# Performance work log

Measured on AMD Instinct MI355X. Metric: run time of the kernel, lower is better.

The kernel has to match this reference:

```python
import jax, jax.numpy as jnp
import numpy as np

DIM = 512
NUM_HEADS = 8
HEAD_DIM = DIM // NUM_HEADS
SCALE = HEAD_DIM ** -0.5
B, N = 8, 1024


def setup_inputs() -> dict:
    key = jax.random.key(0)
    k1, k2, k3, k4, k5 = jax.random.split(key, 5)
    x = jax.random.normal(k1, (B, N, DIM), dtype=jnp.float32)
    rpe_bias = jax.random.normal(k2, (1, NUM_HEADS, N, N), dtype=jnp.float32)
    # torch Linear weights: [out_features, in_features], y = x @ W.T
    qkv_w = jax.random.normal(k3, (3 * DIM, DIM), dtype=jnp.float32) * (DIM ** -0.5)
    proj_w = jax.random.normal(k4, (DIM, DIM), dtype=jnp.float32) * (DIM ** -0.5)
    proj_b = jax.random.normal(k5, (DIM,), dtype=jnp.float32) * 0.01
    return {"x": x, "rpe_bias": rpe_bias, "qkv_w": qkv_w, "proj_w": proj_w, "proj_b": proj_b}


def reference(x, rpe_bias, qkv_w, proj_w, proj_b):
    b, n, c = x.shape
    h, d = NUM_HEADS, HEAD_DIM
    # qkv projection (no bias): [B,N,3C] -> [3,B,H,N,D]
    qkv = (x @ qkv_w.T).reshape(b, n, 3, h, d).transpose(2, 0, 3, 1, 4)
    q, k, v = qkv[0], qkv[1], qkv[2]
    attn = jnp.einsum('bhnd,bhmd->bhnm', q, k) * SCALE + rpe_bias
    attn = jax.nn.softmax(attn, axis=-1)  # dropout p=0 -> identity
    out = jnp.einsum('bhnm,bhmd->bhnd', attn, v)
    out = out.transpose(0, 2, 1, 3).reshape(b, n, c)
    return out @ proj_w.T + proj_b
```

## Files before the change

### kernel.cpp

```cpp
#include <hip/hip_runtime.h>
#include <hip/hip_bf16.h>

#define B_    8
#define N_    1024
#define DIM_  512
#define H_    8
#define DH_   64
#define SCALE_ 0.125f

typedef unsigned short u16;
typedef __attribute__((ext_vector_type(8))) short bf16x8;
typedef __attribute__((ext_vector_type(4))) float f32x4;

__device__ __forceinline__ u16 f2bf(float f) {
  union { float f; unsigned u; } v; v.f = f;
  return (u16)((v.u + 0x7fffu + ((v.u >> 16) & 1u)) >> 16);
}
__device__ __forceinline__ unsigned pack2(float a, float b) {
  return (unsigned)f2bf(a) | ((unsigned)f2bf(b) << 16);
}
__device__ __forceinline__ void cp16(const void* g, void* l) {
  __builtin_amdgcn_global_load_lds(
      (const __attribute__((address_space(1))) unsigned*)g,
      (__attribute__((address_space(3))) unsigned*)l, 16, 0, 0);
}

__global__ __launch_bounds__(256) void convert_kernel(
    const float* __restrict__ X, const float* __restrict__ Wq,
    const float* __restrict__ Wp, u16* __restrict__ Xb,
    u16* __restrict__ Wqb, u16* __restrict__ Wpb) {
  const int NX4 = (B_ * N_ * DIM_) / 4;
  const int NQ4 = (3 * DIM_ * DIM_) / 4;
  const int NP4 = (DIM_ * DIM_) / 4;
  const int total = NX4 + NQ4 + NP4;
  const int stride = gridDim.x * 256;
  for (int i = blockIdx.x * 256 + threadIdx.x; i < total; i += stride) {
    const float* s; u16* d; int off;
    if (i < NX4)            { s = X;  d = Xb;  off = i; }
    else if (i < NX4 + NQ4) { s = Wq; d = Wqb; off = i - NX4; }
    else                    { s = Wp; d = Wpb; off = i - NX4 - NQ4; }
    float4 f = *(const float4*)(s + (size_t)off * 4);
    uint2 u; u.x = pack2(f.x, f.y); u.y = pack2(f.z, f.w);
    *(uint2*)(d + (size_t)off * 4) = u;
  }
}

__global__ __launch_bounds__(256) void qkv_gemm(
    const u16* __restrict__ Ab, const u16* __restrict__ Bb,
    u16* __restrict__ Q, u16* __restrict__ K, u16* __restrict__ Vt) {
  __shared__ __align__(16) u16 sA[128 * 64];
  __shared__ __align__(16) u16 sB[128 * 64];
  const int t = threadIdx.x;
  const int wv = t >> 6, lane = t & 63, quad = (lane >> 4) & 3, l15 = lane & 15;
  const int wr = wv >> 1, wc = wv & 1;
  const int m0 = blockIdx.y * 128;
  const int n0 = blockIdx.x * 128;

  const int srow = lane >> 3;
  const int schunk = (lane & 7) ^ srow;
  const size_t ga = (size_t)(m0 + srow) * DIM_ + schunk * 8;
  const size_t gb = (size_t)(n0 + srow) * DIM_ + schunk * 8;

  f32x4 zero = {0.f, 0.f, 0.f, 0.f};
  f32x4 acc[4][4];
#pragma unroll
  for (int i = 0; i < 4; i++)
#pragma unroll
    for (int j = 0; j < 4; j++) acc[i][j] = zero;

  for (int k0 = 0; k0 < DIM_; k0 += 64) {
    __syncthreads();
#pragma unroll
    for (int i = 0; i < 4; i++) {
      const int rb = 32 * wv + 8 * i;
      cp16(Ab + ga + (size_t)rb * DIM_ + k0, &sA[rb * 64]);
      cp16(Bb + gb + (size_t)rb * DIM_ + k0, &sB[rb * 64]);
    }
    __syncthreads();
#pragma unroll
    for (int ks = 0; ks < 2; ks++) {
      bf16x8 af[4], bfv[4];
#pragma unroll
      for (int i = 0; i < 4; i++)
        af[i] = *(const bf16x8*)&sA[(wr * 64 + 16 * i + l15) * 64 +
                                    (((ks << 2) | quad) ^ (l15 & 7)) * 8];
#pragma unroll
      for (int j = 0; j < 4; j++)
        bfv[j] = *(const bf16x8*)&sB[(wc * 64 + 16 * j + l15) * 64 +
                                     (((ks << 2) | quad) ^ (l15 & 7)) * 8];
#pragma unroll
      for (int i = 0; i < 4; i++)
#pragma unroll
        for (int j = 0; j < 4; j++)
          acc[i][j] = __builtin_amdgcn_mfma_f32_16x16x32_bf16(af[i], bfv[j], acc[i][j], 0, 0, 0);
    }
  }

  const int tsel = n0 >> 9;
#pragma unroll
  for (int j = 0; j < 4; j++) {
    const int jg = n0 + wc * 64 + 16 * j + l15;
    const int h = (jg >> 6) & 7, d = jg & 63;
#pragma unroll
    for (int i = 0; i < 4; i++) {
      const int mbase = m0 + wr * 64 + 16 * i + quad * 4;
      const int b = mbase >> 10, nb = mbase & 1023;
      const size_t bh = (size_t)(b * H_ + h);
      if (tsel == 2) {
        ushort4 v4;
        v4.x = f2bf(acc[i][j][0]); v4.y = f2bf(acc[i][j][1]);
        v4.z = f2bf(acc[i][j][2]); v4.w = f2bf(acc[i][j][3]);
        *(ushort4*)&Vt[(bh * DH_ + d) * N_ + nb] = v4;
      } else {
        u16* dst = (tsel == 0 ? Q : K);
#pragma unroll
        for (int rr = 0; rr < 4; rr++)
          dst[(bh * N_ + nb + rr) * DH_ + d] = f2bf(acc[i][j][rr]);
      }
    }
  }
}

__global__ __launch_bounds__(256) void attn_kernel(
    const u16* __restrict__ Q, const u16* __restrict__ K,
    const u16* __restrict__ Vt, const float* __restrict__ bias,
    u16* __restrict__ AO) {
  __shared__ __align__(16) u16 sK[2][64 * 64];
  __shared__ __align__(16) u16 sV[2][64 * 64];
  __shared__ __align__(16) u16 sP[64 * 64];
  const int t = threadIdx.x;
  const int wv = t >> 6, lane = t & 63, quad = (lane >> 4) & 3, l15 = lane & 15;

  const int bid = blockIdx.x;
  const int h = bid & 7;
  const int s = bid >> 3;
  const int nx = s >> 3;
  const int b = s & 7;
  const int n0 = nx << 7;
  const int bh = b * H_ + h;
  const int r = t >> 2, c = (t & 3) << 4;

  const int qgA = n0 + 16 * wv + l15;
  const int qgB = qgA + 64;
  bf16x8 qfA0, qfA1, qfB0, qfB1;
  {
    const u16* qa = Q + (((size_t)bh << 10) + qgA) * DH_ + (quad << 3);
    const u16* qb = Q + (((size_t)bh << 10) + qgB) * DH_ + (quad << 3);
    qfA0 = *(const bf16x8*)qa; qfA1 = *(const bf16x8*)(qa + 32);
    qfB0 = *(const bf16x8*)qb; qfB1 = *(const bf16x8*)(qb + 32);
  }

  const float* bpA = bias + (((size_t)h << 10) + qgA) * N_ + (quad << 2);
  const float* bpB = bias + (((size_t)h << 10) + qgB) * N_ + (quad << 2);
  const u16* kbase = K + (((size_t)bh << 10) + r) * DH_ + c;
  const u16* vbase = Vt + (((size_t)bh << 6) + r) * N_ + c;

  const int so0 = r * 128 + ((((t & 3) << 5)) ^ ((r & 7) << 4));
  const int so1 = r * 128 + ((((t & 3) << 5) + 16) ^ ((r & 7) << 4));
  const int rx = (l15 & 7) << 4;
  const int frow = l15 * 128;
  const int prow = (16 * wv + l15) * 128;

  f32x4 zero = {0.f, 0.f, 0.f, 0.f};
  f32x4 OA[4], OB[4];
#pragma unroll
  for (int i = 0; i < 4; i++) { OA[i] = zero; OB[i] = zero; }
  float lsumA = 0.f, lsumB = 0.f;

  uint4 k0r = *(const uint4*)kbase, k1r = *(const uint4*)(kbase + 8);
  uint4 v0r = *(const uint4*)vbase, v1r = *(const uint4*)(vbase + 8);
  *(uint4*)((char*)sK[0] + so0) = k0r; *(uint4*)((char*)sK[0] + so1) = k1r;
  *(uint4*)((char*)sV[0] + so0) = v0r; *(uint4*)((char*)sV[0] + so1) = v1r;
  {
    const u16* kn = kbase + (size_t)64 * DH_;
    const u16* vn = vbase + 64;
    k0r = *(const uint4*)kn; k1r = *(const uint4*)(kn + 8);
    v0r = *(const uint4*)vn; v1r = *(const uint4*)(vn + 8);
  }
  __syncthreads();

  for (int kt = 0; kt < 16; kt++) {
    const u16* cK = sK[kt & 1];
    const u16* cV = sV[kt & 1];
    if (kt < 15) {
      u16* wK = sK[(kt & 1) ^ 1]; u16* wV = sV[(kt & 1) ^ 1];
      *(uint4*)((char*)wK + so0) = k0r; *(uint4*)((char*)wK + so1) = k1r;
      *(uint4*)((char*)wV + so0) = v0r; *(uint4*)((char*)wV + so1) = v1r;
      if (kt < 14) {
        const u16* kn = kbase + (size_t)(kt + 2) * 64 * DH_;
        const u16* vn = vbase + (kt + 2) * 64;
        k0r = *(const uint4*)kn; k1r = *(const uint4*)(kn + 8);
        v0r = *(const uint4*)vn; v1r = *(const uint4*)(vn + 8);
      }
    }
    float4 bA[4], bB[4];
#pragma unroll
    for (int cb = 0; cb < 4; cb++) {
      bA[cb] = *(const float4*)(bpA + (kt << 6) + 16 * cb);
      bB[cb] = *(const float4*)(bpB + (kt << 6) + 16 * cb);
    }

    bf16x8 kf[8];
#pragma unroll
    for (int ks = 0; ks < 2; ks++)
#pragma unroll
      for (int cb = 0; cb < 4; cb++)
        kf[ks * 4 + cb] = *(const bf16x8*)((const char*)cK + cb * 2048 + frow +
                                           (((ks << 6) | (quad << 4)) ^ rx));

    f32x4 SA[4], SB[4];
#pragma unroll
    for (int i = 0; i < 4; i++) { SA[i] = zero; SB[i] = zero; }
    __builtin_amdgcn_s_setprio(1);
#pragma unroll
    for (int ks = 0; ks < 2; ks++) {
      const bf16x8 qa = ks ? qfA1 : qfA0;
      const bf16x8 qb = ks ? qfB1 : qfB0;
#pragma unroll
      for (int cb = 0; cb < 4; cb++) {
        SA[cb] = __builtin_amdgcn_mfma_f32_16x16x32_bf16(kf[ks * 4 + cb], qa, SA[cb], 0, 0, 0);
        SB[cb] = __builtin_amdgcn_mfma_f32_16x16x32_bf16(kf[ks * 4 + cb], qb, SB[cb], 0, 0, 0);
      }
    }
    __builtin_amdgcn_s_setprio(0);

#pragma unroll
    for (int cb = 0; cb < 4; cb++) {
      float p0 = __expf(fmaf(SA[cb][0], SCALE_, bA[cb].x));
      float p1 = __expf(fmaf(SA[cb][1], SCALE_, bA[cb].y));
      float p2 = __expf(fmaf(SA[cb][2], SCALE_, bA[cb].z));
      float p3 = __expf(fmaf(SA[cb][3], SCALE_, bA[cb].w));
      lsumA += (p0 + p1) + (p2 + p3);
      uint2 pk; pk.x = pack2(p0, p1); pk.y = pack2(p2, p3);
      *(uint2*)((char*)sP + prow + (((cb << 5) | (quad << 3)) ^ rx)) = pk;
    }
    bf16x8 vf[8];
#pragma unroll
    for (int ks = 0; ks < 2; ks++)
#pragma unroll
      for (int cb = 0; cb < 4; cb++)
        vf[ks * 4 + cb] = *(const bf16x8*)((const char*)cV + cb * 2048 + frow +
                                           (((ks << 6) | (quad << 4)) ^ rx));
    asm volatile("s_waitcnt lgkmcnt(0)" ::: "memory");

    __builtin_amdgcn_s_setprio(1);
#pragma unroll
    for (int ks = 0; ks < 2; ks++) {
      bf16x8 pf = *(const bf16x8*)((const char*)sP + prow +
                                   (((ks << 6) | (quad << 4)) ^ rx));
#pragma unroll
      for (int cb = 0; cb < 4; cb++)
        OA[cb] = __builtin_amdgcn_mfma_f32_16x16x32_bf16(vf[ks * 4 + cb], pf, OA[cb], 0, 0, 0);
    }
    __builtin_amdgcn_s_setprio(0);

#pragma unroll
    for (int cb = 0; cb < 4; cb++) {
      float p0 = __expf(fmaf(SB[cb][0], SCALE_, bB[cb].x));
      float p1 = __expf(fmaf(SB[cb][1], SCALE_, bB[cb].y));
      float p2 = __expf(fmaf(SB[cb][2], SCALE_, bB[cb].z));
      float p3 = __expf(fmaf(SB[cb][3], SCALE_, bB[cb].w));
      lsumB += (p0 + p1) + (p2 + p3);
      uint2 pk; pk.x = pack2(p0, p1); pk.y = pack2(p2, p3);
      *(uint2*)((char*)sP + prow + (((cb << 5) | (quad << 3)) ^ rx)) = pk;
    }
    asm volatile("s_waitcnt lgkmcnt(0)" ::: "memory");
    __builtin_amdgcn_s_setprio(1);
#pragma unroll
    for (int ks = 0; ks < 2; ks++) {
      bf16x8 pf = *(const bf16x8*)((const char*)sP + prow +
                                   (((ks << 6) | (quad << 4)) ^ rx));
#pragma unroll
      for (int cb = 0; cb < 4; cb++)
        OB[cb] = __builtin_amdgcn_mfma_f32_16x16x32_bf16(vf[ks * 4 + cb], pf, OB[cb], 0, 0, 0);
    }
    __builtin_amdgcn_s_setprio(0);
    __syncthreads();
  }

  lsumA += __shfl_xor(lsumA, 16); lsumA += __shfl_xor(lsumA, 32);
  lsumB += __shfl_xor(lsumB, 16); lsumB += __shfl_xor(lsumB, 32);
  const float invA = 1.f / lsumA, invB = 1.f / lsumB;
#pragma unroll
  for (int cb = 0; cb < 4; cb++) {
    ushort4 o4;
    o4.x = f2bf(OA[cb][0] * invA); o4.y = f2bf(OA[cb][1] * invA);
    o4.z = f2bf(OA[cb][2] * invA); o4.w = f2bf(OA[cb][3] * invA);
    *(ushort4*)&AO[(((size_t)b << 10) + qgA) * DIM_ + h * DH_ + 16 * cb + (quad << 2)] = o4;
    ushort4 p4;
    p4.x = f2bf(OB[cb][0] * invB); p4.y = f2bf(OB[cb][1] * invB);
    p4.z = f2bf(OB[cb][2] * invB); p4.w = f2bf(OB[cb][3] * invB);
    *(ushort4*)&AO[(((size_t)b << 10) + qgB) * DIM_ + h * DH_ + 16 * cb + (quad << 2)] = p4;
  }
}

__global__ __launch_bounds__(256) void proj_gemm(
    const u16* __restrict__ Ab, const u16* __restrict__ Bb,
    const float* __restrict__ Pb, float* __restrict__ Out) {
  __shared__ __align__(16) u16 sA[128 * 64];
  __shared__ __align__(16) u16 sB[128 * 64];
  const int t = threadIdx.x;
  const int wv = t >> 6, lane = t & 63, quad = (lane >> 4) & 3, l15 = lane & 15;
  const int wr = wv >> 1, wc = wv & 1;
  const int m0 = blockIdx.y * 128;
  const int n0 = blockIdx.x * 128;

  const int srow = lane >> 3;
  const int schunk = (lane & 7) ^ srow;
  const size_t ga = (size_t)(m0 + srow) * DIM_ + schunk * 8;
  const size_t gb = (size_t)(n0 + srow) * DIM_ + schunk * 8;

  f32x4 zero = {0.f, 0.f, 0.f, 0.f};
  f32x4 acc[4][4];
#pragma unroll
  for (int i = 0; i < 4; i++)
#pragma unroll
    for (int j = 0; j < 4; j++) acc[i][j] = zero;

  for (int k0 = 0; k0 < DIM_; k0 += 64) {
    __syncthreads();
#pragma unroll
    for (int i = 0; i < 4; i++) {
      const int rb = 32 * wv + 8 * i;
      cp16(Ab + ga + (size_t)rb * DIM_ + k0, &sA[rb * 64]);
      cp16(Bb + gb + (size_t)rb * DIM_ + k0, &sB[rb * 64]);
    }
    __syncthreads();
#pragma unroll
    for (int ks = 0; ks < 2; ks++) {
      bf16x8 af[4], bfv[4];
#pragma unroll
      for (int i = 0; i < 4; i++)
        af[i] = *(const bf16x8*)&sA[(wr * 64 + 16 * i + l15) * 64 +
                                    (((ks << 2) | quad) ^ (l15 & 7)) * 8];
#pragma unroll
      for (int j = 0; j < 4; j++)
        bfv[j] = *(const bf16x8*)&sB[(wc * 64 + 16 * j + l15) * 64 +
                                     (((ks << 2) | quad) ^ (l15 & 7)) * 8];
#pragma unroll
      for (int i = 0; i < 4; i++)
#pragma unroll
        for (int j = 0; j < 4; j++)
          acc[i][j] = __builtin_amdgcn_mfma_f32_16x16x32_bf16(af[i], bfv[j], acc[i][j], 0, 0, 0);
    }
  }

#pragma unroll
  for (int j = 0; j < 4; j++) {
    const int jg = n0 + wc * 64 + 16 * j + l15;
    const float pb = Pb[jg];
#pragma unroll
    for (int i = 0; i < 4; i++) {
      const int mbase = m0 + wr * 64 + 16 * i + quad * 4;
#pragma unroll
      for (int rr = 0; rr < 4; rr++)
        Out[(size_t)(mbase + rr) * DIM_ + jg] = acc[i][j][rr] + pb;
    }
  }
}

extern "C" void kernel_launch(void* const* d_in, const int* in_sizes, int n_in,
                              void* d_out, int out_size, void* d_ws, size_t ws_size,
                              hipStream_t stream) {
  const float* x      = (const float*)d_in[0];
  const float* rpe    = (const float*)d_in[1];
  const float* qkv_w  = (const float*)d_in[2];
  const float* proj_w = (const float*)d_in[3];
  const float* proj_b = (const float*)d_in[4];
  float* out = (float*)d_out;

  const size_t perbuf = (size_t)B_ * N_ * DIM_;
  u16* Xb  = (u16*)d_ws;
  u16* Q   = Xb + perbuf;
  u16* K   = Q + perbuf;
  u16* Vt  = K + perbuf;
  u16* Wqb = Vt + perbuf;
  u16* Wpb = Wqb + (size_t)3 * DIM_ * DIM_;
  u16* AO  = Xb;

  convert_kernel<<<2560, 256, 0, stream>>>(x, qkv_w, proj_w, Xb, Wqb, Wpb);
  qkv_gemm<<<dim3(12, 64), 256, 0, stream>>>(Xb, Wqb, Q, K, Vt);
  attn_kernel<<<512, 256, 0, stream>>>(Q, K, Vt, rpe, AO);
  proj_gemm<<<dim3(4, 64), 256, 0, stream>>>(AO, Wpb, proj_b, out);
}
```

Baseline: 177.3 us.

## Keep softmax probabilities in registers, feeding PV MFMA directly without LDS round-trip

Drops the shared-memory P buffer and its write/read round-trip with waits. The QK^T accumulator layout is reused directly as the B operand of 16x16x16 bf16 MFMAs, and the V fragments are re-read from LDS as 4-element slices matching that layout. This removes LDS traffic and synchronisation, but doubles the PV MFMA instruction count (smaller K per instruction) and adds more, smaller V LDS reads and register pressure.

```diff
diff --git a/kernel.cpp b/kernel.cpp
--- a/kernel.cpp
+++ b/kernel.cpp
@@ -10,6 +10,7 @@
 
 typedef unsigned short u16;
 typedef __attribute__((ext_vector_type(8))) short bf16x8;
+typedef __attribute__((ext_vector_type(4))) short bf16x4;
 typedef __attribute__((ext_vector_type(4))) float f32x4;
 
 __device__ __forceinline__ u16 f2bf(float f) {
@@ -127,7 +128,6 @@
     u16* __restrict__ AO) {
   __shared__ __align__(16) u16 sK[2][64 * 64];
   __shared__ __align__(16) u16 sV[2][64 * 64];
-  __shared__ __align__(16) u16 sP[64 * 64];
   const int t = threadIdx.x;
   const int wv = t >> 6, lane = t & 63, quad = (lane >> 4) & 3, l15 = lane & 15;
 
@@ -159,7 +159,7 @@
   const int so1 = r * 128 + ((((t & 3) << 5) + 16) ^ ((r & 7) << 4));
   const int rx = (l15 & 7) << 4;
   const int frow = l15 * 128;
-  const int prow = (16 * wv + l15) * 128;
+  const int vhalf = (quad & 1) << 3;
 
   f32x4 zero = {0.f, 0.f, 0.f, 0.f};
   f32x4 OA[4], OB[4];
@@ -224,6 +224,17 @@
     }
     __builtin_amdgcn_s_setprio(0);
 
+    bf16x4 vf2[4][4];
+#pragma unroll
+    for (int cbp = 0; cbp < 4; cbp++)
+#pragma unroll
+      for (int cb = 0; cb < 4; cb++) {
+        const int ch = ((((2 * cb + (quad >> 1)) << 4)) ^ rx) + vhalf;
+        vf2[cbp][cb] =
+            *(const bf16x4*)((const char*)cV + cbp * 2048 + frow + ch);
+      }
+
+    bf16x4 pA[4], pB[4];
 #pragma unroll
     for (int cb = 0; cb < 4; cb++) {
       float p0 = __expf(fmaf(SA[cb][0], SCALE_, bA[cb].x));
@@ -232,26 +243,15 @@
       float p3 = __expf(fmaf(SA[cb][3], SCALE_, bA[cb].w));
       lsumA += (p0 + p1) + (p2 + p3);
       uint2 pk; pk.x = pack2(p0, p1); pk.y = pack2(p2, p3);
-      *(uint2*)((char*)sP + prow + (((cb << 5) | (quad << 3)) ^ rx)) = pk;
-    }
-    bf16x8 vf[8];
-#pragma unroll
-    for (int ks = 0; ks < 2; ks++)
+      pA[cb] = __builtin_bit_cast(bf16x4, pk);
+    }
+
+    __builtin_amdgcn_s_setprio(1);
+#pragma unroll
+    for (int cbp = 0; cbp < 4; cbp++)
 #pragma unroll
       for (int cb = 0; cb < 4; cb++)
-        vf[ks * 4 + cb] = *(const bf16x8*)((const char*)cV + cb * 2048 + frow +
-                                           (((ks << 6) | (quad << 4)) ^ rx));
-    asm volatile("s_waitcnt lgkmcnt(0)" ::: "memory");
-
-    __builtin_amdgcn_s_setprio(1);
-#pragma unroll
-    for (int ks = 0; ks < 2; ks++) {
-      bf16x8 pf = *(const bf16x8*)((const char*)sP + prow +
-                                   (((ks << 6) | (quad << 4)) ^ rx));
-#pragma unroll
-      for (int cb = 0; cb < 4; cb++)
-        OA[cb] = __builtin_amdgcn_mfma_f32_16x16x32_bf16(vf[ks * 4 + cb], pf, OA[cb], 0, 0, 0);
-    }
+        OA[cbp] = __builtin_amdgcn_mfma_f32_16x16x16bf16_1k(vf2[cbp][cb], pA[cb], OA[cbp], 0, 0, 0);
     __builtin_amdgcn_s_setprio(0);
 
 #pragma unroll
@@ -262,18 +262,14 @@
       float p3 = __expf(fmaf(SB[cb][3], SCALE_, bB[cb].w));
       lsumB += (p0 + p1) + (p2 + p3);
       uint2 pk; pk.x = pack2(p0, p1); pk.y = pack2(p2, p3);
-      *(uint2*)((char*)sP + prow + (((cb << 5) | (quad << 3)) ^ rx)) = pk;
-    }
-    asm volatile("s_waitcnt lgkmcnt(0)" ::: "memory");
+      pB[cb] = __builtin_bit_cast(bf16x4, pk);
+    }
     __builtin_amdgcn_s_setprio(1);
 #pragma unroll
-    for (int ks = 0; ks < 2; ks++) {
-      bf16x8 pf = *(const bf16x8*)((const char*)sP + prow +
-                                   (((ks << 6) | (quad << 4)) ^ rx));
+    for (int cbp = 0; cbp < 4; cbp++)
 #pragma unroll
       for (int cb = 0; cb < 4; cb++)
-        OB[cb] = __builtin_amdgcn_mfma_f32_16x16x32_bf16(vf[ks * 4 + cb], pf, OB[cb], 0, 0, 0);
-    }
+        OB[cbp] = __builtin_amdgcn_mfma_f32_16x16x16bf16_1k(vf2[cbp][cb], pB[cb], OB[cbp], 0, 0, 0);
     __builtin_amdgcn_s_setprio(0);
     __syncthreads();
   }
```

After: 177.2 us. Within noise of the previous version (-0.1%).
